# Performance work log

Hardware: AMD Instinct MI355X
Metric: run time of the kernel (lower is better)

## Reference

```python
import jax, jax.numpy as jnp
import numpy as np
import math

B, S, D, H, V = 2, 2048, 512, 4, 32000
WINDOWS = [None, 128, 512, None]  # per-head attention windows (None = unlimited)


def setup_inputs() -> dict:
    key = jax.random.key(0)
    ks = jax.random.split(key, 8)
    input_ids = jax.random.randint(ks[0], (B, S), 0, V, dtype=jnp.int64)
    padding_mask = jnp.zeros((B, S), dtype=bool)  # True = pad
    embed_table = jax.random.normal(ks[1], (V, D), dtype=jnp.float32) * 0.02
    self_factors = jnp.full((H,), 0.1, dtype=jnp.float32)
    distance_alphas = jnp.full((H,), 0.1, dtype=jnp.float32)
    # torch Linear weights: [out_features, in_features], xavier-uniform init
    lim_f = math.sqrt(6.0 / (H * D + D))
    fusion_w = jax.random.uniform(ks[2], (D, H * D), jnp.float32, -lim_f, lim_f)
    fusion_b = jnp.zeros((D,), jnp.float32)
    lim_o = math.sqrt(6.0 / (D + V))
    out_w = jax.random.uniform(ks[3], (V, D), jnp.float32, -lim_o, lim_o)
    out_b = jnp.zeros((V,), jnp.float32)
    return {
        "input_ids": input_ids,
        "padding_mask": padding_mask,
        "embed_table": embed_table,
        "self_factors": self_factors,
        "distance_alphas": distance_alphas,
        "fusion_w": fusion_w,
        "fusion_b": fusion_b,
        "out_w": out_w,
        "out_b": out_b,
    }


def reference(input_ids, padding_mask, embed_table, self_factors,
              distance_alphas, fusion_w, fusion_b, out_w, out_b):
    b, s = input_ids.shape
    d = embed_table.shape[1]
    h = self_factors.shape[0]

    emb = embed_table[input_ids]  # [B,S,D]

    pos = jnp.arange(s)
    dist = jnp.abs(pos[:, None] - pos[None, :])          # [S,S]
    causal = pos[None, :] > pos[:, None]                  # [S,S] strict upper triangle
    eye = dist == 0                                       # [S,S]

    # shared raw scores, computed once (same for all heads)
    base = jnp.einsum('bqd,bkd->bqk', emb, emb) / math.sqrt(d)  # [B,S,S]

    # per-head distance decay bias: [H,S,S]
    decay = 1.0 / (1.0 + distance_alphas[:, None, None] * dist.astype(jnp.float32))

    scores = base[None, :, :, :] * decay[:, None, :, :]   # [H,B,S,S]
    # diagonal self-factor scaling
    scores = jnp.where(eye[None, None],
                       scores * self_factors[:, None, None, None], scores)

    # per-head window mask (None -> window >= S, never masks)
    win = jnp.array([s if w is None else w for w in WINDOWS[:h]])
    window_mask = dist[None, :, :] > win[:, None, None]   # [H,S,S]

    # key padding mask, diagonal exempted (as in original)
    key_pad = padding_mask[:, None, :] & (~eye[None])      # [B,S,S]

    full_mask = (window_mask[:, None] | causal[None, None] | key_pad[None])  # [H,B,S,S]
    scores = jnp.where(full_mask, -jnp.inf, scores)

    attn = jax.nn.softmax(scores, axis=-1)                 # [H,B,S,S]
    ctx = jnp.einsum('hbqk,bkd->hbqd', attn, emb)          # [H,B,S,D]

    concat = jnp.moveaxis(ctx, 0, 2).reshape(b, s, h * d)  # [B,S,H*D]
    fused = concat @ fusion_w.T + fusion_b                 # [B,S,D]
    logits = fused @ out_w.T + out_b                       # [B,S,V]
    return logits
```

## Files before the change

kernel.cpp:

```cpp
#include <hip/hip_runtime.h>
#include <hip/hip_bf16.h>
#include <stdint.h>

#define BB 2
#define SB 2048
#define DD 512
#define HH 4
#define VV 32000

typedef __attribute__((ext_vector_type(4))) float f32x4;
typedef __attribute__((ext_vector_type(8))) short bf16x8;
typedef __attribute__((ext_vector_type(4))) unsigned short us4;

__device__ __forceinline__ unsigned short f2bf(float f) {
    unsigned u = __float_as_uint(f);
    u += 0x7fffu + ((u >> 16) & 1u);
    return (unsigned short)(u >> 16);
}

__device__ __forceinline__ __attribute__((address_space(3))) unsigned int*
as_lds(void* p) {
    return (__attribute__((address_space(3))) unsigned int*)(unsigned)(uintptr_t)p;
}
__device__ __forceinline__ const __attribute__((address_space(1))) unsigned int*
as_gbl(const void* p) {
    return (const __attribute__((address_space(1))) unsigned int*)(uintptr_t)p;
}

__device__ __forceinline__ bf16x8 ldsrd64(const unsigned short* base, int row, int c) {
    return *(const bf16x8*)((const char*)base + row * 128 + ((c ^ (row & 7)) << 4));
}

__global__ void k_prep(const int* __restrict__ ids, const float* __restrict__ tbl,
                       const float* __restrict__ als,
                       const float* __restrict__ fw, const float* __restrict__ ow,
                       unsigned short* __restrict__ outw_bf, unsigned short* __restrict__ fusw_bf,
                       unsigned short* __restrict__ emb, unsigned short* __restrict__ embT,
                       float* __restrict__ dtab, float* __restrict__ lsum)
{
    __shared__ unsigned short TT[64][72];
    const int bid = blockIdx.x, t = threadIdx.x;

    if (bid < 2000) {
        int base = bid * 8192 + t * 4;
#pragma unroll
        for (int it = 0; it < 8; ++it) {
            int i = base + it * 1024;
            float4 v = *(const float4*)(ow + i);
            us4 o; o.x = f2bf(v.x); o.y = f2bf(v.y); o.z = f2bf(v.z); o.w = f2bf(v.w);
            *(us4*)(outw_bf + i) = o;
        }
    } else if (bid < 2256) {
        int base = (bid - 2000) * 4096 + t * 4;
#pragma unroll
        for (int it = 0; it < 4; ++it) {
            int i = base + it * 1024;
            float4 v = *(const float4*)(fw + i);
            us4 o; o.x = f2bf(v.x); o.y = f2bf(v.y); o.z = f2bf(v.z); o.w = f2bf(v.w);
            *(us4*)(fusw_bf + i) = o;
        }
    } else if (bid < 6352) {
        int row = bid - 2256;
        int id = ids[row];
        if (id < 0) id = 0;
        if (id >= VV) id = VV - 1;
        const float* s = tbl + (size_t)id * DD;
        unsigned short* d = emb + (size_t)row * DD;
        d[t]       = f2bf(s[t]);
        d[t + 256] = f2bf(s[t + 256]);
    } else if (bid < 6448) {
        int i = (bid - 6352) * 256 + t;
        if (i < HH * SB) {
            int h = i >> 11, dd = i & (SB - 1);
            dtab[i] = 0.04419417382415922f / (1.f + als[h] * (float)dd);
        } else {
            lsum[i - HH * SB] = 0.f;
        }
    } else {
        int bid2 = bid - 6448;
        const int d0 = (bid2 & 7) * 64, s0 = ((bid2 >> 3) & 31) * 64, b = bid2 >> 8;
        {
            int s = t >> 2, c16 = (t & 3) * 16;
            int id = ids[b * SB + s0 + s];
            if (id < 0) id = 0;
            if (id >= VV) id = VV - 1;
            const float* src = tbl + (size_t)id * DD + d0 + c16;
#pragma unroll
            for (int q4 = 0; q4 < 4; ++q4) {
                float4 v = *(const float4*)(src + q4 * 4);
                TT[c16 + q4 * 4 + 0][s] = f2bf(v.x);
                TT[c16 + q4 * 4 + 1][s] = f2bf(v.y);
                TT[c16 + q4 * 4 + 2][s] = f2bf(v.z);
                TT[c16 + q4 * 4 + 3][s] = f2bf(v.w);
            }
        }
        __syncthreads();
        {
            int d = t >> 2, sc = (t & 3) * 16;
            bf16x8 o0, o1;
#pragma unroll
            for (int j = 0; j < 8; ++j) {
                o0[j] = (short)TT[d][sc + j];
                o1[j] = (short)TT[d][sc + 8 + j];
            }
            unsigned short* dst = embT + ((size_t)(b * DD + d0 + d)) * SB + s0 + sc;
            *(bf16x8*)dst = o0;
            *(bf16x8*)(dst + 8) = o1;
        }
    }
}

__launch_bounds__(256, 2)
__global__ void k_base(const unsigned short* __restrict__ emb,
                       const unsigned char* __restrict__ pad,
                       const float* __restrict__ sfs,
                       const float* __restrict__ dtab,
                       unsigned short* __restrict__ P,
                       float* __restrict__ lsum)
{
    const int kt = blockIdx.x, qt = blockIdx.y, b = blockIdx.z;
    if (kt > qt + 1) return;
    const int tid = threadIdx.x, lane = tid & 63, wv = tid >> 6;
    const int l15 = lane & 15, g = lane >> 4;

    if (kt == qt + 1) {
        int row = tid >> 2, cb = (tid & 3) * 16;
        int4 z = {0, 0, 0, 0};
#pragma unroll
        for (int h = 0; h < 4; ++h) {
            unsigned short* Ph = P + (((size_t)(h * 2 + b)) * SB + qt * 64 + row) * SB + kt * 64 + cb;
            *(int4*)Ph = z;
            *(int4*)(Ph + 8) = z;
        }
        return;
    }

    __shared__ __align__(16) unsigned short Ql[64 * 128];
    __shared__ __align__(16) unsigned short Kl[64 * 128];

    const int q = qt * 64 + wv * 16 + l15;

    f32x4 zero4 = {0.f, 0.f, 0.f, 0.f};
    f32x4 cc[4];
#pragma unroll
    for (int c = 0; c < 4; ++c) cc[c] = zero4;

    for (int dc = 0; dc < 4; ++dc) {
        const int d0 = dc * 128;
        __syncthreads();
#pragma unroll
        for (int i = 0; i < 4; ++i) {
            int flat = (i * 256 + tid) * 8;
            int row = flat >> 7;
            int ch  = (flat >> 3) & 15;
            int scol = ((ch ^ (row & 15)) << 3);
            __builtin_amdgcn_global_load_lds(
                as_gbl(emb + ((size_t)(b * SB + qt * 64 + row)) * DD + d0 + scol),
                as_lds(Ql + flat), 16, 0, 0);
            __builtin_amdgcn_global_load_lds(
                as_gbl(emb + ((size_t)(b * SB + kt * 64 + row)) * DD + d0 + scol),
                as_lds(Kl + flat), 16, 0, 0);
        }
        asm volatile("s_waitcnt vmcnt(0)" ::: "memory");
        __syncthreads();

#pragma unroll
        for (int dsl = 0; dsl < 4; ++dsl) {
            int chr = (dsl * 4 + g);
            bf16x8 qf = *(const bf16x8*)(Ql + (wv * 16 + l15) * 128 + ((chr ^ l15) << 3));
#pragma unroll
            for (int c = 0; c < 4; ++c) {
                bf16x8 kf = *(const bf16x8*)(Kl + (c * 16 + l15) * 128 + ((chr ^ l15) << 3));
                cc[c] = __builtin_amdgcn_mfma_f32_16x16x32_bf16(kf, qf, cc[c], 0, 0, 0);
            }
        }
    }

    unsigned long long padm = __ballot(pad[(size_t)b * SB + kt * 64 + lane] != 0);

    const int wins[4] = {1 << 30, 128, 512, 1 << 30};
#pragma unroll
    for (int h = 0; h < 4; ++h) {
        const int win = wins[h];
        if (kt * 64 + win + 192 < qt * 64) continue;
        const float sf = sfs[h];
        const float* dth = dtab + h * SB;
        float rsum = 0.f;
        unsigned short pb[4][4];
#pragma unroll
        for (int c = 0; c < 4; ++c) {
#pragma unroll
            for (int r = 0; r < 4; ++r) {
                int kk = kt * 64 + c * 16 + 4 * g + r;
                int dist = q - kk;
                float p = 0.f;
                if (dist >= 0 && dist <= win &&
                    ((dist == 0) || !((padm >> (c * 16 + 4 * g + r)) & 1ull))) {
                    float s = cc[c][r] * dth[dist];
                    if (dist == 0) s *= sf;
                    p = __expf(s);
                }
                rsum += p;
                pb[c][r] = f2bf(p);
            }
        }
        unsigned short* Ph = P + (((size_t)(h * 2 + b)) * SB + q) * SB + kt * 64;
#pragma unroll
        for (int c = 0; c < 4; ++c) {
            us4 o;
            o.x = pb[c][0]; o.y = pb[c][1]; o.z = pb[c][2]; o.w = pb[c][3];
            *(us4*)(Ph + c * 16 + 4 * g) = o;
        }
        rsum += __shfl_xor(rsum, 16, 64);
        rsum += __shfl_xor(rsum, 32, 64);
        if (lane < 16)
            atomicAdd(&lsum[((size_t)(h * 2 + b)) * SB + q], rsum);
    }
}

__launch_bounds__(256, 2)
__global__ void k_pv(const unsigned short* __restrict__ P,
                     const unsigned short* __restrict__ embT,
                     const float* __restrict__ lsum,
                     unsigned short* __restrict__ concat)
{
    const int t64 = blockIdx.x, b = blockIdx.y, h = blockIdx.z;
    const int mt = t64 >> 2, nt = t64 & 3;
    const int Q0 = mt * 128;
    const int win = (h == 1) ? 128 : (h == 2) ? 512 : (1 << 30);
    int klo = Q0 - win - 64; if (klo < 0) klo = 0; klo &= ~63;
    const int khi = Q0 + 128;

    __shared__ __align__(16) unsigned short Al[128 * 32];
    __shared__ __align__(16) unsigned short Bl[128 * 32];

    const int tid = threadIdx.x, lane = tid & 63, wv = tid >> 6;
    const int wm = (wv >> 1) * 64, wn = (wv & 1) * 64;
    const int l15 = lane & 15, g = lane >> 4;

    f32x4 zero4 = {0.f, 0.f, 0.f, 0.f};
    f32x4 acc[4][4];
#pragma unroll
    for (int i = 0; i < 4; ++i)
#pragma unroll
        for (int j = 0; j < 4; ++j) acc[i][j] = zero4;

    const unsigned short* Ab = P + (((size_t)(h * 2 + b)) * SB + Q0) * SB;
    const unsigned short* Bb = embT + ((size_t)(b * DD + nt * 128)) * SB;

    for (int k0 = klo; k0 < khi; k0 += 32) {
        __syncthreads();
#pragma unroll
        for (int s = 0; s < 2; ++s) {
            int e = (s * 256 + tid) * 8;
            int row = e >> 5, col = e & 31;
            __builtin_amdgcn_global_load_lds(as_gbl(Ab + (size_t)row * SB + k0 + col),
                                             as_lds(Al + e), 16, 0, 0);
            __builtin_amdgcn_global_load_lds(as_gbl(Bb + (size_t)row * SB + k0 + col),
                                             as_lds(Bl + e), 16, 0, 0);
        }
        asm volatile("s_waitcnt vmcnt(0)" ::: "memory");
        __syncthreads();

        bf16x8 af[4], bfr[4];
#pragma unroll
        for (int i = 0; i < 4; ++i) {
            af[i]  = *(const bf16x8*)(Al + (wm + i * 16 + l15) * 32 + 8 * g);
            bfr[i] = *(const bf16x8*)(Bl + (wn + i * 16 + l15) * 32 + 8 * g);
        }
#pragma unroll
        for (int i = 0; i < 4; ++i)
#pragma unroll
            for (int j = 0; j < 4; ++j)
                acc[i][j] = __builtin_amdgcn_mfma_f32_16x16x32_bf16(af[i], bfr[j], acc[i][j], 0, 0, 0);
    }

    const float* ls = lsum + ((size_t)(h * 2 + b)) * SB;
    unsigned short* cb = concat + ((size_t)(b * SB)) * (HH * DD) + h * DD + nt * 128;
#pragma unroll
    for (int i = 0; i < 4; ++i) {
        int rowb = wm + i * 16 + g * 4;
        float inv[4];
#pragma unroll
        for (int rr = 0; rr < 4; ++rr) inv[rr] = 1.f / ls[Q0 + rowb + rr];
#pragma unroll
        for (int j = 0; j < 4; ++j) {
            int col = wn + j * 16 + l15;
#pragma unroll
            for (int rr = 0; rr < 4; ++rr)
                cb[(size_t)(Q0 + rowb + rr) * (HH * DD) + col] = f2bf(acc[i][j][rr] * inv[rr]);
        }
    }
}

template <int OUTF32>
__launch_bounds__(256, 2)
__global__ void k_gemm_bt(const unsigned short* __restrict__ A,
                          const unsigned short* __restrict__ Bt,
                          const float* __restrict__ bias,
                          void* __restrict__ Cout,
                          int M, int N, int K)
{
    const int nMt = M >> 7;
    const int nwg = gridDim.x;
    int bid = blockIdx.x;
    int q = nwg >> 3, r = nwg & 7;
    int x = bid & 7, o = bid >> 3;
    int wg = (x < r ? x * (q + 1) : r * (q + 1) + (x - r) * q) + o;
    const int mt = wg % nMt, nt = wg / nMt;

    __shared__ __align__(16) unsigned short Al[128 * 32];
    __shared__ __align__(16) unsigned short Bl[128 * 32];

    const int tid = threadIdx.x;
    const int lane = tid & 63;
    const int wv = tid >> 6;
    const int wm = (wv >> 1) * 64, wn = (wv & 1) * 64;
    const int l15 = lane & 15, g = lane >> 4;

    f32x4 zero4 = {0.f, 0.f, 0.f, 0.f};
    f32x4 acc[4][4];
#pragma unroll
    for (int i = 0; i < 4; ++i)
#pragma unroll
        for (int j = 0; j < 4; ++j) acc[i][j] = zero4;

    const unsigned short* Ab = A + (size_t)mt * 128 * K;
    const unsigned short* Bb = Bt + (size_t)nt * 128 * K;

    for (int k0 = 0; k0 < K; k0 += 32) {
        __syncthreads();
#pragma unroll
        for (int s = 0; s < 2; ++s) {
            int e = (s * 256 + tid) * 8;
            int row = e >> 5, col = e & 31;
            __builtin_amdgcn_global_load_lds(as_gbl(Ab + (size_t)row * K + k0 + col),
                                             as_lds(Al + e), 16, 0, 0);
            __builtin_amdgcn_global_load_lds(as_gbl(Bb + (size_t)row * K + k0 + col),
                                             as_lds(Bl + e), 16, 0, 0);
        }
        asm volatile("s_waitcnt vmcnt(0)" ::: "memory");
        __syncthreads();

        bf16x8 af[4], bfr[4];
#pragma unroll
        for (int i = 0; i < 4; ++i) {
            af[i]  = *(const bf16x8*)(Al + (wm + i * 16 + l15) * 32 + 8 * g);
            bfr[i] = *(const bf16x8*)(Bl + (wn + i * 16 + l15) * 32 + 8 * g);
        }
#pragma unroll
        for (int i = 0; i < 4; ++i)
#pragma unroll
            for (int j = 0; j < 4; ++j)
                acc[i][j] = __builtin_amdgcn_mfma_f32_16x16x32_bf16(af[i], bfr[j], acc[i][j], 0, 0, 0);
    }

#pragma unroll
    for (int i = 0; i < 4; ++i) {
        int rowb = mt * 128 + wm + i * 16 + g * 4;
#pragma unroll
        for (int j = 0; j < 4; ++j) {
            int col = nt * 128 + wn + j * 16 + l15;
            float bv = bias[col];
            if (OUTF32) {
                float* C = (float*)Cout;
#pragma unroll
                for (int rr = 0; rr < 4; ++rr)
                    C[(size_t)(rowb + rr) * N + col] = acc[i][j][rr] + bv;
            } else {
                unsigned short* C = (unsigned short*)Cout;
#pragma unroll
                for (int rr = 0; rr < 4; ++rr)
                    C[(size_t)(rowb + rr) * N + col] = f2bf(acc[i][j][rr] + bv);
            }
        }
    }
}

__launch_bounds__(512, 1)
__global__ void k_logits(const unsigned short* __restrict__ A,
                         const unsigned short* __restrict__ Bt,
                         const float* __restrict__ bias,
                         float* __restrict__ Cout,
                         int M, int N, int K)
{
    const int nMt = M >> 8;
    const int nwg = gridDim.x;
    int bid = blockIdx.x;
    int q = nwg >> 3, r = nwg & 7;
    int x = bid & 7, o = bid >> 3;
    int wg = (x < r ? x * (q + 1) : r * (q + 1) + (x - r) * q) + o;
    const int mt = wg % nMt, nt = wg / nMt;

    __shared__ __align__(16) unsigned short Al[2][256 * 64];
    __shared__ __align__(16) unsigned short Bl[2][256 * 64];

    const int tid = threadIdx.x, lane = tid & 63, wv = tid >> 6;
    const int wr = wv >> 2, wc = wv & 3;
    const int l15 = lane & 15, g = lane >> 4;

    f32x4 zero4 = {0.f, 0.f, 0.f, 0.f};
    f32x4 acc[8][4];
#pragma unroll
    for (int i = 0; i < 8; ++i)
#pragma unroll
        for (int j = 0; j < 4; ++j) acc[i][j] = zero4;

    const unsigned short* Ab = A + (size_t)mt * 256 * K;
    const unsigned short* Bb = Bt + (size_t)nt * 256 * K;

    const unsigned short* As[4];
    const unsigned short* Bs[4];
    int ldst[4];
#pragma unroll
    for (int j = 0; j < 4; ++j) {
        int ch = tid + j * 512;
        int row = ch >> 3, cpos = ch & 7;
        int scol = ((cpos ^ (row & 7)) << 3);
        As[j] = Ab + (size_t)row * K + scol;
        Bs[j] = Bb + (size_t)row * K + scol;
        ldst[j] = ch * 8;
    }

#define STG(bufi_, k0_) {                                                         \
    _Pragma("unroll")                                                             \
    for (int j = 0; j < 4; ++j)                                                   \
        __builtin_amdgcn_global_load_lds(as_gbl(As[j] + (k0_)),                   \
                                         as_lds(&Al[bufi_][ldst[j]]), 16, 0, 0);  \
    _Pragma("unroll")                                                             \
    for (int j = 0; j < 4; ++j)                                                   \
        __builtin_amdgcn_global_load_lds(as_gbl(Bs[j] + (k0_)),                   \
                                         as_lds(&Bl[bufi_][ldst[j]]), 16, 0, 0); }

    STG(0, 0);
    __syncthreads();

    for (int t = 0; t < 8; ++t) {
        const int cur = t & 1;
        if (t < 7) STG(cur ^ 1, (t + 1) * 64);
        const unsigned short* Ar = Al[cur];
        const unsigned short* Br = Bl[cur];
#pragma unroll
        for (int s = 0; s < 2; ++s) {
            bf16x8 bf[4], af[8];
#pragma unroll
            for (int n = 0; n < 4; ++n)
                bf[n] = ldsrd64(Br, wc * 64 + n * 16 + l15, s * 4 + g);
#pragma unroll
            for (int m = 0; m < 8; ++m)
                af[m] = ldsrd64(Ar, wr * 128 + m * 16 + l15, s * 4 + g);
            __builtin_amdgcn_s_setprio(1);
#pragma unroll
            for (int m = 0; m < 8; ++m)
#pragma unroll
                for (int n = 0; n < 4; ++n)
                    acc[m][n] = __builtin_amdgcn_mfma_f32_16x16x32_bf16(af[m], bf[n], acc[m][n], 0, 0, 0);
            __builtin_amdgcn_s_setprio(0);
        }
        __syncthreads();
    }
#undef STG

    const int mrow = mt * 256 + wr * 128;
    const int ncol = nt * 256 + wc * 64;
#pragma unroll
    for (int i = 0; i < 8; ++i) {
        int rowb = mrow + i * 16 + g * 4;
#pragma unroll
        for (int j = 0; j < 4; ++j) {
            int col = ncol + j * 16 + l15;
            float bv = bias[col];
#pragma unroll
            for (int rr = 0; rr < 4; ++rr)
                Cout[(size_t)(rowb + rr) * N + col] = acc[i][j][rr] + bv;
        }
    }
}

extern "C" void kernel_launch(void* const* d_in, const int* in_sizes, int n_in,
                              void* d_out, int out_size, void* d_ws, size_t ws_size,
                              hipStream_t stream)
{
    const int*           ids = (const int*)d_in[0];
    const unsigned char* pad = (const unsigned char*)d_in[1];
    const float*         tbl = (const float*)d_in[2];
    const float*         sfs = (const float*)d_in[3];
    const float*         als = (const float*)d_in[4];
    const float*         fw  = (const float*)d_in[5];
    const float*         fb  = (const float*)d_in[6];
    const float*         ow  = (const float*)d_in[7];
    const float*         ob  = (const float*)d_in[8];
    float* logits = (float*)d_out;

    char* ws = (char*)d_ws;
    unsigned short* outw_bf = (unsigned short*)(ws);
    unsigned short* fusw_bf = (unsigned short*)(ws + 32768000);
    unsigned short* emb_bf  = (unsigned short*)(ws + 34865152);
    unsigned short* concat  = (unsigned short*)(ws + 39059456);
    unsigned short* fused   = (unsigned short*)(ws + 55836672);

    char* ob_scratch = (char*)d_out;
    unsigned short* P    = (unsigned short*)(ob_scratch);
    unsigned short* embT = (unsigned short*)(ob_scratch + 67108864);
    float*          dtab = (float*)(ob_scratch + 71303168);
    float*          lsum = (float*)(ob_scratch + 71335936);

    k_prep<<<6960, 256, 0, stream>>>(ids, tbl, als, fw, ow,
                                     outw_bf, fusw_bf, emb_bf, embT, dtab, lsum);

    dim3 bg(32, 32, BB);
    k_base<<<bg, 256, 0, stream>>>(emb_bf, pad, sfs, dtab, P, lsum);

    dim3 pg(64, BB, HH);
    k_pv<<<pg, 256, 0, stream>>>(P, embT, lsum, concat);

    k_gemm_bt<0><<<32 * 4, 256, 0, stream>>>(concat, fusw_bf, fb, fused, BB * SB, DD, HH * DD);
    k_logits<<<16 * 125, 512, 0, stream>>>(fused, outw_bf, ob, logits, BB * SB, VV, DD);
}
```

Baseline: 379.6 us.

## Retile logits GEMM to 512x128 with K32 stages for two blocks per CU

Changes the output-projection GEMM tile from 256x256 with 64-wide K steps to a 512x128 tile with 32-wide K steps. LDS use drops to 80KB so two workgroups can share a CU, and the launch bound now asks for two blocks per CU. The aim is more latency hiding and overlap of staging with compute. The cost is twice as many K iterations and barriers, and a tighter register budget. With a 128-float accumulator per thread, that budget could force spills.

```diff
diff --git a/kernel.cpp b/kernel.cpp
--- a/kernel.cpp
+++ b/kernel.cpp
@@ -25,10 +25,6 @@
 __device__ __forceinline__ const __attribute__((address_space(1))) unsigned int*
 as_gbl(const void* p) {
     return (const __attribute__((address_space(1))) unsigned int*)(uintptr_t)p;
-}
-
-__device__ __forceinline__ bf16x8 ldsrd64(const unsigned short* base, int row, int c) {
-    return *(const bf16x8*)((const char*)base + row * 128 + ((c ^ (row & 7)) << 4));
 }
 
 __global__ void k_prep(const int* __restrict__ ids, const float* __restrict__ tbl,
@@ -377,14 +373,14 @@
     }
 }
 
-__launch_bounds__(512, 1)
+__launch_bounds__(512, 2)
 __global__ void k_logits(const unsigned short* __restrict__ A,
                          const unsigned short* __restrict__ Bt,
                          const float* __restrict__ bias,
                          float* __restrict__ Cout,
                          int M, int N, int K)
 {
-    const int nMt = M >> 8;
+    const int nMt = M >> 9;
     const int nwg = gridDim.x;
     int bid = blockIdx.x;
     int q = nwg >> 3, r = nwg & 7;
@@ -392,11 +388,10 @@
     int wg = (x < r ? x * (q + 1) : r * (q + 1) + (x - r) * q) + o;
     const int mt = wg % nMt, nt = wg / nMt;
 
-    __shared__ __align__(16) unsigned short Al[2][256 * 64];
-    __shared__ __align__(16) unsigned short Bl[2][256 * 64];
+    __shared__ __align__(16) char smem[81920];
 
     const int tid = threadIdx.x, lane = tid & 63, wv = tid >> 6;
-    const int wr = wv >> 2, wc = wv & 3;
+    const int wr = wv >> 1, wc = wv & 1;
     const int l15 = lane & 15, g = lane >> 4;
 
     f32x4 zero4 = {0.f, 0.f, 0.f, 0.f};
@@ -406,63 +401,69 @@
 #pragma unroll
         for (int j = 0; j < 4; ++j) acc[i][j] = zero4;
 
-    const unsigned short* Ab = A + (size_t)mt * 256 * K;
-    const unsigned short* Bb = Bt + (size_t)nt * 256 * K;
+    const unsigned short* Ab = A + (size_t)mt * 512 * K;
+    const unsigned short* Bb = Bt + (size_t)nt * 128 * K;
 
     const unsigned short* As[4];
-    const unsigned short* Bs[4];
-    int ldst[4];
+    int ldstA[4];
 #pragma unroll
     for (int j = 0; j < 4; ++j) {
         int ch = tid + j * 512;
-        int row = ch >> 3, cpos = ch & 7;
-        int scol = ((cpos ^ (row & 7)) << 3);
+        int row = ch >> 2, p = ch & 3;
+        int scol = ((p ^ (row & 3)) << 3);
         As[j] = Ab + (size_t)row * K + scol;
-        Bs[j] = Bb + (size_t)row * K + scol;
-        ldst[j] = ch * 8;
-    }
-
-#define STG(bufi_, k0_) {                                                         \
-    _Pragma("unroll")                                                             \
-    for (int j = 0; j < 4; ++j)                                                   \
-        __builtin_amdgcn_global_load_lds(as_gbl(As[j] + (k0_)),                   \
-                                         as_lds(&Al[bufi_][ldst[j]]), 16, 0, 0);  \
-    _Pragma("unroll")                                                             \
-    for (int j = 0; j < 4; ++j)                                                   \
-        __builtin_amdgcn_global_load_lds(as_gbl(Bs[j] + (k0_)),                   \
-                                         as_lds(&Bl[bufi_][ldst[j]]), 16, 0, 0); }
+        ldstA[j] = ch * 16;
+    }
+    const unsigned short* Bsrc;
+    int ldstB;
+    {
+        int row = tid >> 2, p = tid & 3;
+        int scol = ((p ^ (row & 3)) << 3);
+        Bsrc = Bb + (size_t)row * K + scol;
+        ldstB = 65536 + tid * 16;
+    }
+
+#define STG(bufi_, k0_) {                                                                   \
+    _Pragma("unroll")                                                                       \
+    for (int j = 0; j < 4; ++j)                                                             \
+        __builtin_amdgcn_global_load_lds(as_gbl(As[j] + (k0_)),                             \
+            as_lds(smem + (bufi_) * 32768 + ldstA[j]), 16, 0, 0);                           \
+    __builtin_amdgcn_global_load_lds(as_gbl(Bsrc + (k0_)),                                  \
+        as_lds(smem + (bufi_) * 8192 + ldstB), 16, 0, 0); }
 
     STG(0, 0);
     __syncthreads();
 
-    for (int t = 0; t < 8; ++t) {
+    for (int t = 0; t < 16; ++t) {
         const int cur = t & 1;
-        if (t < 7) STG(cur ^ 1, (t + 1) * 64);
-        const unsigned short* Ar = Al[cur];
-        const unsigned short* Br = Bl[cur];
-#pragma unroll
-        for (int s = 0; s < 2; ++s) {
-            bf16x8 bf[4], af[8];
+        if (t < 15) STG(cur ^ 1, (t + 1) * 32);
+        const unsigned short* Ar = (const unsigned short*)(smem + cur * 32768);
+        const unsigned short* Br = (const unsigned short*)(smem + 65536 + cur * 8192);
+
+        bf16x8 bf[4], af[8];
+#pragma unroll
+        for (int n = 0; n < 4; ++n) {
+            int row = wc * 64 + n * 16 + l15;
+            bf[n] = *(const bf16x8*)((const char*)Br + row * 64 + ((g ^ (row & 3)) << 4));
+        }
+#pragma unroll
+        for (int m = 0; m < 8; ++m) {
+            int row = wr * 128 + m * 16 + l15;
+            af[m] = *(const bf16x8*)((const char*)Ar + row * 64 + ((g ^ (row & 3)) << 4));
+        }
+        __builtin_amdgcn_s_setprio(1);
+#pragma unroll
+        for (int m = 0; m < 8; ++m)
 #pragma unroll
             for (int n = 0; n < 4; ++n)
-                bf[n] = ldsrd64(Br, wc * 64 + n * 16 + l15, s * 4 + g);
-#pragma unroll
-            for (int m = 0; m < 8; ++m)
-                af[m] = ldsrd64(Ar, wr * 128 + m * 16 + l15, s * 4 + g);
-            __builtin_amdgcn_s_setprio(1);
-#pragma unroll
-            for (int m = 0; m < 8; ++m)
-#pragma unroll
-                for (int n = 0; n < 4; ++n)
-                    acc[m][n] = __builtin_amdgcn_mfma_f32_16x16x32_bf16(af[m], bf[n], acc[m][n], 0, 0, 0);
-            __builtin_amdgcn_s_setprio(0);
-        }
+                acc[m][n] = __builtin_amdgcn_mfma_f32_16x16x32_bf16(af[m], bf[n], acc[m][n], 0, 0, 0);
+        __builtin_amdgcn_s_setprio(0);
         __syncthreads();
     }
 #undef STG
 
-    const int mrow = mt * 256 + wr * 128;
-    const int ncol = nt * 256 + wc * 64;
+    const int mrow = mt * 512 + wr * 128;
+    const int ncol = nt * 128 + wc * 64;
 #pragma unroll
     for (int i = 0; i < 8; ++i) {
         int rowb = mrow + i * 16 + g * 4;
@@ -515,5 +516,5 @@
     k_pv<<<pg, 256, 0, stream>>>(P, embT, lsum, concat);
 
     k_gemm_bt<0><<<32 * 4, 256, 0, stream>>>(concat, fusw_bf, fb, fused, BB * SB, DD, HH * DD);
-    k_logits<<<16 * 125, 512, 0, stream>>>(fused, outw_bf, ob, logits, BB * SB, VV, DD);
-}
+    k_logits<<<8 * 250, 512, 0, stream>>>(fused, outw_bf, ob, logits, BB * SB, VV, DD);
+}
```

Result: slower. 389.0 us (+2.5%).
